# Kernel optimization log

Hardware: AMD Instinct MI355X
Metric: run time of the kernel (lower is better)

The kernel has to match this reference:

```python
import jax, jax.numpy as jnp
import numpy as np

B, N, L = 2, 2048, 2048
DQ, DKV, H, WF = 1024, 1024, 16, 4
HD = DQ // H
EPS = 1e-5


def _ln(x, g, b):
    m = jnp.mean(x, axis=-1, keepdims=True)
    v = jnp.mean(jnp.square(x - m), axis=-1, keepdims=True)
    return (x - m) * jax.lax.rsqrt(v + EPS) * g + b


def setup_inputs() -> dict:
    key = jax.random.key(0)
    ks = jax.random.split(key, 12)
    s = 0.02
    return {
        "x_q": jax.random.normal(ks[0], (B, N, DQ), jnp.float32),
        "x_kv": jax.random.normal(ks[1], (B, L, DKV), jnp.float32),
        "qn_g": jnp.ones((DQ,), jnp.float32),
        "qn_b": jnp.zeros((DQ,), jnp.float32),
        "kvn_g": jnp.ones((DKV,), jnp.float32),
        "kvn_b": jnp.zeros((DKV,), jnp.float32),
        "Wq": jax.random.normal(ks[2], (DQ, DQ), jnp.float32) * s,
        "bq": jnp.zeros((DQ,), jnp.float32),
        "Wk": jax.random.normal(ks[3], (DQ, DKV), jnp.float32) * s,
        "bk": jnp.zeros((DQ,), jnp.float32),
        "Wv": jax.random.normal(ks[4], (DQ, DKV), jnp.float32) * s,
        "bv": jnp.zeros((DQ,), jnp.float32),
        "Wo": jax.random.normal(ks[5], (DQ, DQ), jnp.float32) * s,
        "bo": jnp.zeros((DQ,), jnp.float32),
        "n2_g": jnp.ones((DQ,), jnp.float32),
        "n2_b": jnp.zeros((DQ,), jnp.float32),
        "W1": jax.random.normal(ks[6], (WF * DQ, DQ), jnp.float32) * s,
        "b1": jnp.zeros((WF * DQ,), jnp.float32),
        "W2": jax.random.normal(ks[7], (DQ, WF * DQ), jnp.float32) * s,
        "b2": jnp.zeros((DQ,), jnp.float32),
    }


def reference(x_q, x_kv, qn_g, qn_b, kvn_g, kvn_b, Wq, bq, Wk, bk, Wv, bv,
              Wo, bo, n2_g, n2_b, W1, b1, W2, b2):
    # projections (torch Linear: x @ W.T + b)
    q = (_ln(x_q, qn_g, qn_b) @ Wq.T + bq).reshape(B, N, H, HD)
    kvn = _ln(x_kv, kvn_g, kvn_b)
    k = (kvn @ Wk.T + bk).reshape(B, L, H, HD)
    v = (kvn @ Wv.T + bv).reshape(B, L, H, HD)

    # attention with softmax-1: exp(s)/(1 + sum exp(s)), numerically stable
    scale = 1.0 / jnp.sqrt(jnp.float32(HD))
    s = jnp.einsum("bnhd,blhd->bhnl", q, k) * scale  # [B,H,N,L]
    m = jnp.max(s, axis=-1, keepdims=True)
    m = jnp.maximum(m, 0.0)  # include the implicit zero logit of softmax-1
    p = jnp.exp(s - m)
    denom = jnp.sum(p, axis=-1, keepdims=True) + jnp.exp(-m)
    attn = p / denom
    attn_out = jnp.einsum("bhnl,blhd->bnhd", attn, v).reshape(B, N, DQ)

    # residual + out proj
    x = x_q + (attn_out @ Wo.T + bo)
    # residual MLP (GELU, exact/erf as torch nn.GELU default)
    h = jax.nn.gelu(_ln(x, n2_g, n2_b) @ W1.T + b1, approximate=False)
    x = x + (h @ W2.T + b2)
    return x
```

## Files before the change

### kernel.cpp

```cpp
#include <hip/hip_runtime.h>
#include <hip/hip_bf16.h>
#include <stdint.h>

#define DEV __device__ __forceinline__

typedef unsigned short ushort_t;
typedef __attribute__((ext_vector_type(8))) short bf16x8;
typedef __attribute__((ext_vector_type(4))) float f32x4;

DEV uint32_t f2bf2(float lo, float hi) {
  uint32_t d;
  asm("v_cvt_pk_bf16_f32 %0, %1, %2" : "=v"(d) : "v"(lo), "v"(hi));
  return d;
}
DEV ushort_t f2bf(float f) { return (ushort_t)f2bf2(f, f); }

DEV void gload_lds16(const void* gp, void* lp) {
  __builtin_amdgcn_global_load_lds(
      (__attribute__((address_space(1))) void*)(void*)(uintptr_t)gp,
      (__attribute__((address_space(3))) void*)lp, 16, 0, 0);
}

__global__ __launch_bounds__(256) void cvt_all(
    const float* __restrict__ Wq, const float* __restrict__ Wk,
    const float* __restrict__ Wv, const float* __restrict__ Wo,
    const float* __restrict__ W1, const float* __restrict__ W2,
    ushort_t* __restrict__ WqB, ushort_t* __restrict__ WKVB,
    ushort_t* __restrict__ WoB, ushort_t* __restrict__ W1B,
    ushort_t* __restrict__ W2B) {
  int i = blockIdx.x * 256 + threadIdx.x;
  const float* src; ushort_t* dst; int j;
  if (i < 262144)            { src = Wq; dst = WqB;           j = i; }
  else if (i < 524288)       { src = Wk; dst = WKVB;          j = i - 262144; }
  else if (i < 786432)       { src = Wv; dst = WKVB + 1048576; j = i - 524288; }
  else if (i < 1048576)      { src = Wo; dst = WoB;           j = i - 786432; }
  else if (i < 2097152)      { src = W1; dst = W1B;           j = i - 1048576; }
  else                       { src = W2; dst = W2B;           j = i - 2097152; }
  float4 v = ((const float4*)src)[j];
  uint2 o; o.x = f2bf2(v.x, v.y); o.y = f2bf2(v.z, v.w);
  ((uint2*)dst)[j] = o;
}

DEV void ln_row(const float* __restrict__ x, const float* __restrict__ g,
                const float* __restrict__ be, ushort_t* __restrict__ out, int row) {
  const int t = threadIdx.x;
  const float4 v = ((const float4*)(x + (size_t)row * 1024))[t];
  float s = v.x + v.y + v.z + v.w;
  float sq = v.x * v.x + v.y * v.y + v.z * v.z + v.w * v.w;
#pragma unroll
  for (int d = 1; d < 64; d <<= 1) { s += __shfl_xor(s, d); sq += __shfl_xor(sq, d); }
  __shared__ float sm[8];
  const int w = t >> 6, lane = t & 63;
  if (lane == 0) { sm[w * 2] = s; sm[w * 2 + 1] = sq; }
  __syncthreads();
  s = sm[0] + sm[2] + sm[4] + sm[6];
  sq = sm[1] + sm[3] + sm[5] + sm[7];
  const float mean = s * (1.f / 1024.f);
  const float var = sq * (1.f / 1024.f) - mean * mean;
  const float rstd = rsqrtf(var + 1e-5f);
  const float4 gv = ((const float4*)g)[t];
  const float4 bv = ((const float4*)be)[t];
  uint2 o;
  o.x = f2bf2((v.x - mean) * rstd * gv.x + bv.x, (v.y - mean) * rstd * gv.y + bv.y);
  o.y = f2bf2((v.z - mean) * rstd * gv.z + bv.z, (v.w - mean) * rstd * gv.w + bv.w);
  ((uint2*)(out + (size_t)row * 1024))[t] = o;
}

__global__ __launch_bounds__(256) void ln_bf16(const float* __restrict__ x,
                                               const float* __restrict__ g,
                                               const float* __restrict__ be,
                                               ushort_t* __restrict__ out) {
  ln_row(x, g, be, out, blockIdx.x);
}

__global__ __launch_bounds__(256) void ln_fused(
    const float* __restrict__ x_q, const float* __restrict__ x_kv,
    const float* __restrict__ qg, const float* __restrict__ qb,
    const float* __restrict__ kg, const float* __restrict__ kb,
    ushort_t* __restrict__ oq, ushort_t* __restrict__ okv) {
  const int r = blockIdx.x;
  if (r < 4096) ln_row(x_q, qg, qb, oq, r);
  else ln_row(x_kv, kg, kb, okv, r - 4096);
}

DEV void xcd_remap(int gx, int gy, int& bx, int& by) {
  const int lin = by * gx + bx;
  const int xcd = lin & 7, s = lin >> 3;
  by = xcd * (gy >> 3) + s / gx;
  bx = s % gx;
}

enum { EPI_BF16 = 0, EPI_KV = 1, EPI_RESID = 2, EPI_GELU = 3 };

template <int TN, int EPI>
__global__ __launch_bounds__(256, 2) void gemm_bt(
    const ushort_t* __restrict__ A,
    const ushort_t* __restrict__ Wb,
    const float* __restrict__ bias,
    const float* __restrict__ bias2,
    const float* __restrict__ resid,
    void* __restrict__ outp, void* __restrict__ outp2,
    int M, int N, int K, float oscale) {
  constexpr int NI = (TN == 128) ? 4 : 2;
  constexpr int NB = TN / 32;
  __shared__ ushort_t As[2][128 * 64];
  __shared__ ushort_t Bs[2][TN * 64];
  const int t = threadIdx.x;
  const int w = t >> 6, lane = t & 63;
  const int qd = lane >> 4, ql = lane & 15;
  int bx = blockIdx.x, by = blockIdx.y;
  xcd_remap(gridDim.x, gridDim.y, bx, by);
  const int m0 = by * 128, n0 = bx * TN;
  const int wm = (TN == 128) ? (w >> 1) * 64 : w * 32;
  const int wn = (TN == 128) ? (w & 1) * 64 : 0;
  const int sw = ql & 7;

  const ushort_t* pa[4];
#pragma unroll
  for (int p = 0; p < 4; p++) {
    int n = p * 256 + t, row = n >> 3, c = (n & 7) ^ (row & 7);
    pa[p] = A + (size_t)(m0 + row) * K + c * 8;
  }
  const ushort_t* pb[NB];
#pragma unroll
  for (int p = 0; p < NB; p++) {
    int n = p * 256 + t, row = n >> 3, c = (n & 7) ^ (row & 7);
    pb[p] = Wb + (size_t)(n0 + row) * K + c * 8;
  }

#pragma unroll
  for (int p = 0; p < 4; p++) { gload_lds16(pa[p], &As[0][(p * 256 + t) * 8]); pa[p] += 64; }
#pragma unroll
  for (int p = 0; p < NB; p++) { gload_lds16(pb[p], &Bs[0][(p * 256 + t) * 8]); pb[p] += 64; }
  __syncthreads();

  f32x4 acc[NI][4] = {};
  const int NIT = K >> 6;
  int cur = 0;

  for (int it = 0; it < NIT; ++it) {
    if (it + 1 < NIT) {
#pragma unroll
      for (int p = 0; p < 4; p++) { gload_lds16(pa[p], &As[1 ^ cur][(p * 256 + t) * 8]); pa[p] += 64; }
#pragma unroll
      for (int p = 0; p < NB; p++) { gload_lds16(pb[p], &Bs[1 ^ cur][(p * 256 + t) * 8]); pb[p] += 64; }
    }
    const ushort_t* Ac = As[cur];
    const ushort_t* Bc = Bs[cur];
#pragma unroll
    for (int ks = 0; ks < 2; ks++) {
      bf16x8 af[NI], bf[4];
#pragma unroll
      for (int i = 0; i < NI; i++)
        af[i] = *(const bf16x8*)&Ac[(wm + i * 16 + ql) * 64 + ((ks * 4 + qd) ^ sw) * 8];
#pragma unroll
      for (int j = 0; j < 4; j++)
        bf[j] = *(const bf16x8*)&Bc[(wn + j * 16 + ql) * 64 + ((ks * 4 + qd) ^ sw) * 8];
#pragma unroll
      for (int i = 0; i < NI; i++)
#pragma unroll
        for (int j = 0; j < 4; j++)
          acc[i][j] = __builtin_amdgcn_mfma_f32_16x16x32_bf16(af[i], bf[j], acc[i][j], 0, 0, 0);
    }
    __syncthreads();
    cur ^= 1;
  }

#pragma unroll
  for (int i = 0; i < NI; i++) {
    const int mr = m0 + wm + i * 16 + qd * 4;
#pragma unroll
    for (int j = 0; j < 4; j++) {
      const int col = n0 + wn + j * 16 + ql;
      f32x4 v = acc[i][j];
      if constexpr (EPI == EPI_BF16) {
        const float bb = bias[col];
        ushort_t* o = (ushort_t*)outp;
#pragma unroll
        for (int r = 0; r < 4; r++) o[(size_t)(mr + r) * N + col] = f2bf((v[r] + bb) * oscale);
      } else if constexpr (EPI == EPI_KV) {
        if (col < 1024) {
          const float bb = bias[col];
          ushort_t* o = (ushort_t*)outp;
#pragma unroll
          for (int r = 0; r < 4; r++) o[(size_t)(mr + r) * 1024 + col] = f2bf(v[r] + bb);
        } else {
          const int vc = col - 1024;
          const float bb = bias2[vc];
          const int h = vc >> 6, d = vc & 63;
          const int b = mr >> 11, l0 = mr & 2047;
          uint2 pk;
          pk.x = f2bf2(v[0] + bb, v[1] + bb);
          pk.y = f2bf2(v[2] + bb, v[3] + bb);
          *(uint2*)((ushort_t*)outp2 + ((((size_t)b * 16 + h) * 64 + d) * 2048 + l0)) = pk;
        }
      } else if constexpr (EPI == EPI_RESID) {
        const float bb = bias[col];
        float* o = (float*)outp;
#pragma unroll
        for (int r = 0; r < 4; r++) {
          size_t idx = (size_t)(mr + r) * N + col;
          o[idx] = resid[idx] + v[r] + bb;
        }
      } else {
        const float bb = bias[col];
        ushort_t* o = (ushort_t*)outp;
#pragma unroll
        for (int r = 0; r < 4; r++) {
          float x = v[r] + bb;
          float gx = 0.5f * x * (1.0f + erff(x * 0.70710678118654752f));
          o[(size_t)(mr + r) * N + col] = f2bf(gx);
        }
      }
    }
  }
}

__global__ __launch_bounds__(256, 2) void flash_attn(const ushort_t* __restrict__ Qg,
                                                     const ushort_t* __restrict__ Kg,
                                                     const ushort_t* __restrict__ VTg,
                                                     ushort_t* __restrict__ Og) {
  __shared__ ushort_t QPs[128 * 64];
  __shared__ ushort_t Ks[2][64 * 64];
  __shared__ ushort_t Vs[2][64 * 64];
  const int t = threadIdx.x, w = t >> 6, lane = t & 63;
  const int qd = lane >> 4, ql = lane & 15;
  int bx = blockIdx.x, bh = blockIdx.y;
  xcd_remap(gridDim.x, gridDim.y, bx, bh);
  const int b = bh >> 4, h = bh & 15;
  const int n0 = bx * 128;
  const ushort_t* Qp = Qg + ((size_t)b * 2048 + n0) * 1024 + h * 64;
  const ushort_t* Kp = Kg + (size_t)b * 2048 * 1024 + h * 64;
  const ushort_t* Vp = VTg + (size_t)bh * 64 * 2048;
  const int sw = ql & 7;

  const ushort_t* kp2[2];
  const ushort_t* vp2[2];
#pragma unroll
  for (int p = 0; p < 2; p++) {
    int n = p * 256 + t, row = n >> 3, c = (n & 7) ^ (row & 7);
    kp2[p] = Kp + (size_t)row * 1024 + c * 8;
    vp2[p] = Vp + (size_t)row * 2048 + c * 8;
  }

#pragma unroll
  for (int p = 0; p < 4; p++) {
    int n = p * 256 + t, row = n >> 3, c = (n & 7) ^ (row & 7);
    gload_lds16(Qp + (size_t)row * 1024 + c * 8, &QPs[n * 8]);
  }
#pragma unroll
  for (int p = 0; p < 2; p++) {
    int n = p * 256 + t;
    gload_lds16(kp2[p], &Ks[0][n * 8]);
    gload_lds16(vp2[p], &Vs[0][n * 8]);
    kp2[p] += 64 * 1024;
    vp2[p] += 64;
  }
  __syncthreads();

  bf16x8 aq[2][2];
#pragma unroll
  for (int i = 0; i < 2; i++)
#pragma unroll
    for (int ks = 0; ks < 2; ks++)
      aq[i][ks] = *(const bf16x8*)&QPs[(w * 32 + i * 16 + ql) * 64 + ((ks * 4 + qd) ^ sw) * 8];
  __syncthreads();

  f32x4 accO[2][4] = {};
  float lro2[2] = {0.f, 0.f};

  int cur = 0;
  for (int lt = 0; lt < 32; ++lt) {
    if (lt + 1 < 32) {
#pragma unroll
      for (int p = 0; p < 2; p++) {
        int n = p * 256 + t;
        gload_lds16(kp2[p], &Ks[1 ^ cur][n * 8]);
        gload_lds16(vp2[p], &Vs[1 ^ cur][n * 8]);
        kp2[p] += 64 * 1024;
        vp2[p] += 64;
      }
    }
    const ushort_t* Kc = Ks[cur];
    const ushort_t* Vc = Vs[cur];

    f32x4 accS[4][2] = {};
#pragma unroll
    for (int ks = 0; ks < 2; ks++) {
      bf16x8 bk[4];
#pragma unroll
      for (int j = 0; j < 4; j++)
        bk[j] = *(const bf16x8*)&Kc[(j * 16 + ql) * 64 + ((ks * 4 + qd) ^ sw) * 8];
#pragma unroll
      for (int j = 0; j < 4; j++)
#pragma unroll
        for (int i = 0; i < 2; i++)
          accS[j][i] = __builtin_amdgcn_mfma_f32_16x16x32_bf16(bk[j], aq[i][ks], accS[j][i], 0, 0, 0);
    }

#pragma unroll
    for (int j = 0; j < 4; j++)
#pragma unroll
      for (int i = 0; i < 2; i++) {
        f32x4 p;
#pragma unroll
        for (int r = 0; r < 4; r++) {
          p[r] = __builtin_amdgcn_exp2f(accS[j][i][r]);
          lro2[i] += p[r];
        }
        const int n = w * 32 + i * 16 + ql;
        const int coff = (((j * 2 + (qd >> 1)) ^ sw) << 3) + ((qd & 1) << 2);
        uint2 pk; pk.x = f2bf2(p[0], p[1]); pk.y = f2bf2(p[2], p[3]);
        *(uint2*)&QPs[n * 64 + coff] = pk;
      }

#pragma unroll
    for (int ks = 0; ks < 2; ks++) {
      bf16x8 ap[2], bv[4];
#pragma unroll
      for (int i = 0; i < 2; i++)
        ap[i] = *(const bf16x8*)&QPs[(w * 32 + i * 16 + ql) * 64 + ((ks * 4 + qd) ^ sw) * 8];
#pragma unroll
      for (int jo = 0; jo < 4; jo++)
        bv[jo] = *(const bf16x8*)&Vc[(jo * 16 + ql) * 64 + ((ks * 4 + qd) ^ sw) * 8];
#pragma unroll
      for (int i = 0; i < 2; i++)
#pragma unroll
        for (int jo = 0; jo < 4; jo++)
          accO[i][jo] = __builtin_amdgcn_mfma_f32_16x16x32_bf16(ap[i], bv[jo], accO[i][jo], 0, 0, 0);
    }

    __syncthreads();
    cur ^= 1;
  }

  float dn[2];
#pragma unroll
  for (int i = 0; i < 2; i++) {
    float l = lro2[i];
    l += __shfl_xor(l, 16);
    l += __shfl_xor(l, 32);
    dn[i] = l + 1.0f;
  }

#pragma unroll
  for (int i = 0; i < 2; i++)
#pragma unroll
    for (int r = 0; r < 4; r++) {
      const float inv = 1.0f / __shfl(dn[i], qd * 4 + r);
      const int row = n0 + w * 32 + i * 16 + qd * 4 + r;
#pragma unroll
      for (int jo = 0; jo < 4; jo++)
        Og[((size_t)b * 2048 + row) * 1024 + h * 64 + jo * 16 + ql] =
            f2bf(accO[i][jo][r] * inv);
    }
}

extern "C" void kernel_launch(void* const* d_in, const int* in_sizes, int n_in,
                              void* d_out, int out_size, void* d_ws, size_t ws_size,
                              hipStream_t stream) {
  const float* x_q = (const float*)d_in[0];
  const float* x_kv = (const float*)d_in[1];
  const float* qn_g = (const float*)d_in[2];
  const float* qn_b = (const float*)d_in[3];
  const float* kvn_g = (const float*)d_in[4];
  const float* kvn_b = (const float*)d_in[5];
  const float* Wq = (const float*)d_in[6];
  const float* bq = (const float*)d_in[7];
  const float* Wk = (const float*)d_in[8];
  const float* bk = (const float*)d_in[9];
  const float* Wv = (const float*)d_in[10];
  const float* bv = (const float*)d_in[11];
  const float* Wo = (const float*)d_in[12];
  const float* bo = (const float*)d_in[13];
  const float* n2_g = (const float*)d_in[14];
  const float* n2_b = (const float*)d_in[15];
  const float* W1 = (const float*)d_in[16];
  const float* b1 = (const float*)d_in[17];
  const float* W2 = (const float*)d_in[18];
  const float* b2 = (const float*)d_in[19];

  char* ws = (char*)d_ws;
  const size_t MB = 1ull << 20;
  ushort_t* WqB = (ushort_t*)(ws + 0 * MB);
  ushort_t* WKVB = (ushort_t*)(ws + 2 * MB);
  ushort_t* WoB = (ushort_t*)(ws + 6 * MB);
  ushort_t* W1B = (ushort_t*)(ws + 8 * MB);
  ushort_t* W2B = (ushort_t*)(ws + 16 * MB);
  ushort_t* LNQ = (ushort_t*)(ws + 24 * MB);
  ushort_t* LNKV = (ushort_t*)(ws + 32 * MB);
  ushort_t* Qb = (ushort_t*)(ws + 40 * MB);
  ushort_t* Kb = (ushort_t*)(ws + 48 * MB);
  ushort_t* VTb = (ushort_t*)(ws + 56 * MB);
  ushort_t* AOb = (ushort_t*)(ws + 64 * MB);
  float* Xf = (float*)(ws + 72 * MB);
  ushort_t* LN2 = (ushort_t*)(ws + 88 * MB);
  ushort_t* Hb = (ushort_t*)(ws + 24 * MB);

  const float QSCALE = 0.18033688011112042f;

  cvt_all<<<12288, 256, 0, stream>>>(Wq, Wk, Wv, Wo, W1, W2, WqB, WKVB, WoB, W1B, W2B);
  ln_fused<<<8192, 256, 0, stream>>>(x_q, x_kv, qn_g, qn_b, kvn_g, kvn_b, LNQ, LNKV);

  gemm_bt<64, EPI_BF16><<<dim3(16, 32), 256, 0, stream>>>(
      LNQ, WqB, bq, nullptr, nullptr, Qb, nullptr, 4096, 1024, 1024, QSCALE);
  gemm_bt<128, EPI_KV><<<dim3(16, 32), 256, 0, stream>>>(
      LNKV, WKVB, bk, bv, nullptr, Kb, VTb, 4096, 2048, 1024, 1.0f);

  flash_attn<<<dim3(16, 32), 256, 0, stream>>>(Qb, Kb, VTb, AOb);

  gemm_bt<64, EPI_RESID><<<dim3(16, 32), 256, 0, stream>>>(
      AOb, WoB, bo, nullptr, x_q, Xf, nullptr, 4096, 1024, 1024, 1.0f);
  ln_bf16<<<4096, 256, 0, stream>>>(Xf, n2_g, n2_b, LN2);
  gemm_bt<128, EPI_GELU><<<dim3(32, 32), 256, 0, stream>>>(
      LN2, W1B, b1, nullptr, nullptr, Hb, nullptr, 4096, 4096, 1024, 1.0f);
  gemm_bt<64, EPI_RESID><<<dim3(16, 32), 256, 0, stream>>>(
      Hb, W2B, b2, nullptr, Xf, (float*)d_out, nullptr, 4096, 1024, 4096, 1.0f);
}
```

Before: 378.0 us.

## Fuse Q/K/V projections into one GEMM and add BK=32 tiles with 3-wave occupancy

Merges the separate Q and K/V projection GEMMs into one launch over a concatenated bf16 weight, choosing the A operand per column block and routing the epilogue to Q, K or transposed V. The GEMM template gains a K-tile size parameter. The QKV and W1/GELU GEMMs use BK=32 with a matching LDS swizzle and smaller shared memory. Launch bounds are raised to 3 blocks per CU. The aim is to remove a launch, fill the GPU with one larger grid, and raise occupancy. The risks are more sync overhead per K step with shorter tiles and register pressure under the tighter launch bound.

```diff
diff --git a/kernel.cpp b/kernel.cpp
--- a/kernel.cpp
+++ b/kernel.cpp
@@ -25,17 +25,16 @@
     const float* __restrict__ Wq, const float* __restrict__ Wk,
     const float* __restrict__ Wv, const float* __restrict__ Wo,
     const float* __restrict__ W1, const float* __restrict__ W2,
-    ushort_t* __restrict__ WqB, ushort_t* __restrict__ WKVB,
-    ushort_t* __restrict__ WoB, ushort_t* __restrict__ W1B,
-    ushort_t* __restrict__ W2B) {
+    ushort_t* __restrict__ WQKVB, ushort_t* __restrict__ WoB,
+    ushort_t* __restrict__ W1B, ushort_t* __restrict__ W2B) {
   int i = blockIdx.x * 256 + threadIdx.x;
   const float* src; ushort_t* dst; int j;
-  if (i < 262144)            { src = Wq; dst = WqB;           j = i; }
-  else if (i < 524288)       { src = Wk; dst = WKVB;          j = i - 262144; }
-  else if (i < 786432)       { src = Wv; dst = WKVB + 1048576; j = i - 524288; }
-  else if (i < 1048576)      { src = Wo; dst = WoB;           j = i - 786432; }
-  else if (i < 2097152)      { src = W1; dst = W1B;           j = i - 1048576; }
-  else                       { src = W2; dst = W2B;           j = i - 2097152; }
+  if (i < 262144)            { src = Wq; dst = WQKVB;            j = i; }
+  else if (i < 524288)       { src = Wk; dst = WQKVB + 1048576;  j = i - 262144; }
+  else if (i < 786432)       { src = Wv; dst = WQKVB + 2097152;  j = i - 524288; }
+  else if (i < 1048576)      { src = Wo; dst = WoB;              j = i - 786432; }
+  else if (i < 2097152)      { src = W1; dst = W1B;              j = i - 1048576; }
+  else                       { src = W2; dst = W2B;              j = i - 2097152; }
   float4 v = ((const float4*)src)[j];
   uint2 o; o.x = f2bf2(v.x, v.y); o.y = f2bf2(v.z, v.w);
   ((uint2*)dst)[j] = o;
@@ -90,21 +89,25 @@
   bx = s % gx;
 }
 
-enum { EPI_BF16 = 0, EPI_KV = 1, EPI_RESID = 2, EPI_GELU = 3 };
-
-template <int TN, int EPI>
-__global__ __launch_bounds__(256, 2) void gemm_bt(
+enum { EPI_BF16 = 0, EPI_KV = 1, EPI_RESID = 2, EPI_GELU = 3, EPI_QKV = 4 };
+
+template <int TN, int BK, int EPI>
+__global__ __launch_bounds__(256, 3) void gemm_bt(
     const ushort_t* __restrict__ A,
+    const ushort_t* __restrict__ A2,
     const ushort_t* __restrict__ Wb,
-    const float* __restrict__ bias,
-    const float* __restrict__ bias2,
+    const float* __restrict__ bias, const float* __restrict__ bias2,
+    const float* __restrict__ bias3,
     const float* __restrict__ resid,
-    void* __restrict__ outp, void* __restrict__ outp2,
+    void* __restrict__ outp, void* __restrict__ outp2, void* __restrict__ outp3,
     int M, int N, int K, float oscale) {
   constexpr int NI = (TN == 128) ? 4 : 2;
-  constexpr int NB = TN / 32;
-  __shared__ ushort_t As[2][128 * 64];
-  __shared__ ushort_t Bs[2][TN * 64];
+  constexpr int CH = BK / 8;
+  constexpr int NA = (128 * CH) / 256;
+  constexpr int NBL = (TN * CH) / 256;
+  constexpr int KS = BK / 32;
+  __shared__ ushort_t As[2][128 * BK];
+  __shared__ ushort_t Bs[2][TN * BK];
   const int t = threadIdx.x;
   const int w = t >> 6, lane = t & 63;
   const int qd = lane >> 4, ql = lane & 15;
@@ -113,49 +116,53 @@
   const int m0 = by * 128, n0 = bx * TN;
   const int wm = (TN == 128) ? (w >> 1) * 64 : w * 32;
   const int wn = (TN == 128) ? (w & 1) * 64 : 0;
-  const int sw = ql & 7;
-
-  const ushort_t* pa[4];
-#pragma unroll
-  for (int p = 0; p < 4; p++) {
-    int n = p * 256 + t, row = n >> 3, c = (n & 7) ^ (row & 7);
-    pa[p] = A + (size_t)(m0 + row) * K + c * 8;
-  }
-  const ushort_t* pb[NB];
-#pragma unroll
-  for (int p = 0; p < NB; p++) {
-    int n = p * 256 + t, row = n >> 3, c = (n & 7) ^ (row & 7);
-    pb[p] = Wb + (size_t)(n0 + row) * K + c * 8;
-  }
-
-#pragma unroll
-  for (int p = 0; p < 4; p++) { gload_lds16(pa[p], &As[0][(p * 256 + t) * 8]); pa[p] += 64; }
-#pragma unroll
-  for (int p = 0; p < NB; p++) { gload_lds16(pb[p], &Bs[0][(p * 256 + t) * 8]); pb[p] += 64; }
+  const int sw = (BK == 64) ? (ql & 7) : ((ql >> 1) & 3);
+
+  const ushort_t* Ause = (EPI == EPI_QKV && n0 >= 1024) ? A2 : A;
+
+  const ushort_t* pa[NA];
+#pragma unroll
+  for (int p = 0; p < NA; p++) {
+    int n = p * 256 + t, row = n / CH, c = n % CH;
+    int g = (BK == 64) ? (c ^ (row & 7)) : (c ^ ((row >> 1) & 3));
+    pa[p] = Ause + (size_t)(m0 + row) * K + g * 8;
+  }
+  const ushort_t* pb[NBL];
+#pragma unroll
+  for (int p = 0; p < NBL; p++) {
+    int n = p * 256 + t, row = n / CH, c = n % CH;
+    int g = (BK == 64) ? (c ^ (row & 7)) : (c ^ ((row >> 1) & 3));
+    pb[p] = Wb + (size_t)(n0 + row) * K + g * 8;
+  }
+
+#pragma unroll
+  for (int p = 0; p < NA; p++) { gload_lds16(pa[p], &As[0][(p * 256 + t) * 8]); pa[p] += BK; }
+#pragma unroll
+  for (int p = 0; p < NBL; p++) { gload_lds16(pb[p], &Bs[0][(p * 256 + t) * 8]); pb[p] += BK; }
   __syncthreads();
 
   f32x4 acc[NI][4] = {};
-  const int NIT = K >> 6;
+  const int NIT = K / BK;
   int cur = 0;
 
   for (int it = 0; it < NIT; ++it) {
     if (it + 1 < NIT) {
 #pragma unroll
-      for (int p = 0; p < 4; p++) { gload_lds16(pa[p], &As[1 ^ cur][(p * 256 + t) * 8]); pa[p] += 64; }
-#pragma unroll
-      for (int p = 0; p < NB; p++) { gload_lds16(pb[p], &Bs[1 ^ cur][(p * 256 + t) * 8]); pb[p] += 64; }
+      for (int p = 0; p < NA; p++) { gload_lds16(pa[p], &As[1 ^ cur][(p * 256 + t) * 8]); pa[p] += BK; }
+#pragma unroll
+      for (int p = 0; p < NBL; p++) { gload_lds16(pb[p], &Bs[1 ^ cur][(p * 256 + t) * 8]); pb[p] += BK; }
     }
     const ushort_t* Ac = As[cur];
     const ushort_t* Bc = Bs[cur];
 #pragma unroll
-    for (int ks = 0; ks < 2; ks++) {
+    for (int ks = 0; ks < KS; ks++) {
       bf16x8 af[NI], bf[4];
 #pragma unroll
       for (int i = 0; i < NI; i++)
-        af[i] = *(const bf16x8*)&Ac[(wm + i * 16 + ql) * 64 + ((ks * 4 + qd) ^ sw) * 8];
+        af[i] = *(const bf16x8*)&Ac[(wm + i * 16 + ql) * BK + ((ks * 4 + qd) ^ sw) * 8];
 #pragma unroll
       for (int j = 0; j < 4; j++)
-        bf[j] = *(const bf16x8*)&Bc[(wn + j * 16 + ql) * 64 + ((ks * 4 + qd) ^ sw) * 8];
+        bf[j] = *(const bf16x8*)&Bc[(wn + j * 16 + ql) * BK + ((ks * 4 + qd) ^ sw) * 8];
 #pragma unroll
       for (int i = 0; i < NI; i++)
 #pragma unroll
@@ -178,21 +185,27 @@
         ushort_t* o = (ushort_t*)outp;
 #pragma unroll
         for (int r = 0; r < 4; r++) o[(size_t)(mr + r) * N + col] = f2bf((v[r] + bb) * oscale);
-      } else if constexpr (EPI == EPI_KV) {
+      } else if constexpr (EPI == EPI_QKV) {
         if (col < 1024) {
           const float bb = bias[col];
           ushort_t* o = (ushort_t*)outp;
 #pragma unroll
-          for (int r = 0; r < 4; r++) o[(size_t)(mr + r) * 1024 + col] = f2bf(v[r] + bb);
+          for (int r = 0; r < 4; r++) o[(size_t)(mr + r) * 1024 + col] = f2bf((v[r] + bb) * oscale);
+        } else if (col < 2048) {
+          const int c2 = col - 1024;
+          const float bb = bias2[c2];
+          ushort_t* o = (ushort_t*)outp2;
+#pragma unroll
+          for (int r = 0; r < 4; r++) o[(size_t)(mr + r) * 1024 + c2] = f2bf(v[r] + bb);
         } else {
-          const int vc = col - 1024;
-          const float bb = bias2[vc];
+          const int vc = col - 2048;
+          const float bb = bias3[vc];
           const int h = vc >> 6, d = vc & 63;
           const int b = mr >> 11, l0 = mr & 2047;
           uint2 pk;
           pk.x = f2bf2(v[0] + bb, v[1] + bb);
           pk.y = f2bf2(v[2] + bb, v[3] + bb);
-          *(uint2*)((ushort_t*)outp2 + ((((size_t)b * 16 + h) * 64 + d) * 2048 + l0)) = pk;
+          *(uint2*)((ushort_t*)outp3 + ((((size_t)b * 16 + h) * 64 + d) * 2048 + l0)) = pk;
         }
       } else if constexpr (EPI == EPI_RESID) {
         const float bb = bias[col];
@@ -202,7 +215,7 @@
           size_t idx = (size_t)(mr + r) * N + col;
           o[idx] = resid[idx] + v[r] + bb;
         }
-      } else {
+      } else if constexpr (EPI == EPI_GELU) {
         const float bb = bias[col];
         ushort_t* o = (ushort_t*)outp;
 #pragma unroll
@@ -382,8 +395,7 @@
 
   char* ws = (char*)d_ws;
   const size_t MB = 1ull << 20;
-  ushort_t* WqB = (ushort_t*)(ws + 0 * MB);
-  ushort_t* WKVB = (ushort_t*)(ws + 2 * MB);
+  ushort_t* WQKVB = (ushort_t*)(ws + 0 * MB);
   ushort_t* WoB = (ushort_t*)(ws + 6 * MB);
   ushort_t* W1B = (ushort_t*)(ws + 8 * MB);
   ushort_t* W2B = (ushort_t*)(ws + 16 * MB);
@@ -399,21 +411,22 @@
 
   const float QSCALE = 0.18033688011112042f;
 
-  cvt_all<<<12288, 256, 0, stream>>>(Wq, Wk, Wv, Wo, W1, W2, WqB, WKVB, WoB, W1B, W2B);
+  cvt_all<<<12288, 256, 0, stream>>>(Wq, Wk, Wv, Wo, W1, W2, WQKVB, WoB, W1B, W2B);
   ln_fused<<<8192, 256, 0, stream>>>(x_q, x_kv, qn_g, qn_b, kvn_g, kvn_b, LNQ, LNKV);
 
-  gemm_bt<64, EPI_BF16><<<dim3(16, 32), 256, 0, stream>>>(
-      LNQ, WqB, bq, nullptr, nullptr, Qb, nullptr, 4096, 1024, 1024, QSCALE);
-  gemm_bt<128, EPI_KV><<<dim3(16, 32), 256, 0, stream>>>(
-      LNKV, WKVB, bk, bv, nullptr, Kb, VTb, 4096, 2048, 1024, 1.0f);
+  gemm_bt<128, 32, EPI_QKV><<<dim3(24, 32), 256, 0, stream>>>(
+      LNQ, LNKV, WQKVB, bq, bk, bv, nullptr, Qb, Kb, VTb, 4096, 3072, 1024, QSCALE);
 
   flash_attn<<<dim3(16, 32), 256, 0, stream>>>(Qb, Kb, VTb, AOb);
 
-  gemm_bt<64, EPI_RESID><<<dim3(16, 32), 256, 0, stream>>>(
-      AOb, WoB, bo, nullptr, x_q, Xf, nullptr, 4096, 1024, 1024, 1.0f);
+  gemm_bt<64, 64, EPI_RESID><<<dim3(16, 32), 256, 0, stream>>>(
+      AOb, nullptr, WoB, bo, nullptr, nullptr, x_q, Xf, nullptr, nullptr,
+      4096, 1024, 1024, 1.0f);
   ln_bf16<<<4096, 256, 0, stream>>>(Xf, n2_g, n2_b, LN2);
-  gemm_bt<128, EPI_GELU><<<dim3(32, 32), 256, 0, stream>>>(
-      LN2, W1B, b1, nullptr, nullptr, Hb, nullptr, 4096, 4096, 1024, 1.0f);
-  gemm_bt<64, EPI_RESID><<<dim3(16, 32), 256, 0, stream>>>(
-      Hb, W2B, b2, nullptr, Xf, (float*)d_out, nullptr, 4096, 1024, 4096, 1.0f);
-}
+  gemm_bt<128, 32, EPI_GELU><<<dim3(32, 32), 256, 0, stream>>>(
+      LN2, nullptr, W1B, b1, nullptr, nullptr, nullptr, Hb, nullptr, nullptr,
+      4096, 4096, 1024, 1.0f);
+  gemm_bt<64, 64, EPI_RESID><<<dim3(16, 32), 256, 0, stream>>>(
+      Hb, nullptr, W2B, b2, nullptr, nullptr, Xf, (float*)d_out, nullptr, nullptr,
+      4096, 1024, 4096, 1.0f);
+}
```

Result: faster. 366.6 us (-3.0%).
